# Performance work log

Hardware: AMD Instinct MI355X
Metric: run time of the kernel (lower is better)

Reference implementation:

```python
import jax, jax.numpy as jnp
import numpy as np

N_FFT = 1024
HOP = 256
WIN = 1024
PAD = (WIN - HOP) // 2  # 'same' padding trim
B, NBINS, T = 32, N_FFT // 2 + 1, 2048


def setup_inputs() -> dict:
    key = jax.random.key(0)
    k1, k2 = jax.random.split(key)
    spec_real = jax.random.normal(k1, (B, NBINS, T), dtype=jnp.float32)
    spec_imag = jax.random.normal(k2, (B, NBINS, T), dtype=jnp.float32)
    # Hann window, as used by neural vocoders (periodic hann)
    n = jnp.arange(WIN, dtype=jnp.float32)
    window = 0.5 - 0.5 * jnp.cos(2.0 * jnp.pi * n / WIN)
    return {"spec_real": spec_real, "spec_imag": spec_imag, "window": window}


def reference(spec_real, spec_imag, window):
    spec = jax.lax.complex(spec_real, spec_imag)            # (B, N, T)
    ifft = jnp.fft.irfft(spec, n=N_FFT, axis=1, norm="backward")  # (B, n_fft, T)
    ifft = ifft * window[None, :, None]                     # windowed frames
    b, _, t = spec_real.shape
    out_size = (t - 1) * HOP + WIN
    idx = jnp.arange(t)[None, :] * HOP + jnp.arange(WIN)[:, None]
    y = jnp.zeros((b, out_size), dtype=ifft.dtype).at[:, idx].add(ifft)
    env = jnp.zeros((out_size,), dtype=window.dtype).at[idx].add(
        jnp.broadcast_to(jnp.square(window)[:, None], (WIN, t))
    )
    return y[:, PAD:-PAD] / env[PAD:-PAD]
```

## Files before the change

### kernel.cpp

```cpp
#include <hip/hip_runtime.h>
#include <hip/hip_fp16.h>

#define NBINS 513
#define TFR   2048
#define NB    32
#define WIN   1024
#define HOP   256
#define PADT  384
#define OPB   524288
#define FR    16
#define TILES (TFR / FR)
#define SPAN  (FR * HOP)
#define FSTRIDE 545
#define PIDX(i) ((i) + ((i) >> 4))
#define C45 0.70710678118654752f
#define TWOPI_1024 0.0061359231515425649f
#define SSC   (1.0f / 512.0f * 2.0f / 3.0f)
#define CDLT  0.99998117528260114f
#define SDLT  0.00613588464915448f

__device__ __forceinline__ float2 cadd(float2 a, float2 b){ return make_float2(a.x+b.x, a.y+b.y); }
__device__ __forceinline__ float2 csub(float2 a, float2 b){ return make_float2(a.x-b.x, a.y-b.y); }
__device__ __forceinline__ float2 cmul(float2 a, float2 b){ return make_float2(a.x*b.x - a.y*b.y, a.x*b.y + a.y*b.x); }
__device__ __forceinline__ float2 h2f(__half2 h){ return __half22float2(h); }
__device__ __forceinline__ __half2 f2h(float x, float y){ return __floats2half2_rn(x, y); }

#define BFLY8(u0,u1,u2,u3,u4,u5,u6,u7, v0,v1,v2,v3,v4,v5,v6,v7)            \
    float2 s0=cadd(u0,u4), t0=csub(u0,u4);                                  \
    float2 s1=cadd(u1,u5), t1=csub(u1,u5);                                  \
    float2 s2=cadd(u2,u6), t2=csub(u2,u6);                                  \
    float2 s3=cadd(u3,u7), t3=csub(u3,u7);                                  \
    t1 = make_float2(C45*(t1.x - t1.y),  C45*(t1.x + t1.y));                \
    t2 = make_float2(-t2.y, t2.x);                                          \
    t3 = make_float2(-C45*(t3.x + t3.y), C45*(t3.x - t3.y));                \
    float2 p0=cadd(s0,s2), p2=csub(s0,s2);                                  \
    float2 p1=cadd(s1,s3), p3=csub(s1,s3); p3 = make_float2(-p3.y, p3.x);   \
    float2 q0=cadd(t0,t2), q2=csub(t0,t2);                                  \
    float2 q1=cadd(t1,t3), q3=csub(t1,t3); q3 = make_float2(-q3.y, q3.x);   \
    float2 v0=cadd(p0,p1), v4=csub(p0,p1);                                  \
    float2 v2=cadd(p2,p3), v6=csub(p2,p3);                                  \
    float2 v1=cadd(q0,q1), v5=csub(q0,q1);                                  \
    float2 v3=cadd(q2,q3), v7=csub(q2,q3);

template<int L>
__device__ __forceinline__ void fft_stage(__half2* __restrict__ row,
                                          const float2* __restrict__ ph, int i)
{
    const int k    = i & (L - 1);
    const int base = ((i & ~(L - 1)) << 3) + k;
    float2 u0 = h2f(row[PIDX(base + 0*L)]);
    float2 u1 = h2f(row[PIDX(base + 1*L)]);
    float2 u2 = h2f(row[PIDX(base + 2*L)]);
    float2 u3 = h2f(row[PIDX(base + 3*L)]);
    float2 u4 = h2f(row[PIDX(base + 4*L)]);
    float2 u5 = h2f(row[PIDX(base + 5*L)]);
    float2 u6 = h2f(row[PIDX(base + 6*L)]);
    float2 u7 = h2f(row[PIDX(base + 7*L)]);
    BFLY8(u0,u1,u2,u3,u4,u5,u6,u7, v0,v1,v2,v3,v4,v5,v6,v7)
    if constexpr (L > 1) {
        const float2 w1 = ph[k * (128 / L)];
        float2 wq = w1;
        v1 = cmul(v1, wq);
        wq = cmul(wq, w1); v2 = cmul(v2, wq);
        wq = cmul(wq, w1); v3 = cmul(v3, wq);
        wq = cmul(wq, w1); v4 = cmul(v4, wq);
        wq = cmul(wq, w1); v5 = cmul(v5, wq);
        wq = cmul(wq, w1); v6 = cmul(v6, wq);
        wq = cmul(wq, w1); v7 = cmul(v7, wq);
    }
    row[PIDX(base + 0*L)] = f2h(v0.x, v0.y);
    row[PIDX(base + 1*L)] = f2h(v1.x, v1.y);
    row[PIDX(base + 2*L)] = f2h(v2.x, v2.y);
    row[PIDX(base + 3*L)] = f2h(v3.x, v3.y);
    row[PIDX(base + 4*L)] = f2h(v4.x, v4.y);
    row[PIDX(base + 5*L)] = f2h(v5.x, v5.y);
    row[PIDX(base + 6*L)] = f2h(v6.x, v6.y);
    row[PIDX(base + 7*L)] = f2h(v7.x, v7.y);
}

__device__ __forceinline__ float2 hann_pair(const float2* __restrict__ ph, int n)
{
    const bool mir = n > 256;
    const int  m   = mir ? 512 - n : n;
    const float2 cs = ph[m];
    const float c = mir ? -cs.x : cs.x;
    const float s = cs.y;
    const float w0 = 1.0f - c*c;
    const float c2 = 2.0f*c*c - 1.0f;
    const float s2 = 2.0f*c*s;
    const float w1 = 0.5f - 0.5f*(c2*CDLT - s2*SDLT);
    return make_float2(w0, w1);
}

__global__ __launch_bounds__(256) void zero_seams(float* __restrict__ out)
{
    const int total = NB * (TILES + 1) * 768;
    for (int id = blockIdx.x * 256 + threadIdx.x; id < total; id += gridDim.x * 256) {
        const int q = id % 768;
        const int r = id / 768;
        const int s = r % (TILES + 1);
        const int bb = r / (TILES + 1);
        const int p  = s * SPAN + q;
        const int oi = p - PADT;
        if ((unsigned)oi < (unsigned)OPB) out[(size_t)bb * OPB + oi] = 0.f;
    }
}

__global__ __launch_bounds__(256, 4) void istft16(
    const float* __restrict__ sr, const float* __restrict__ si,
    float* __restrict__ out)
{
    __shared__ __half2 stile[FR * FSTRIDE];
    __shared__ float2  ph[257];

    const int tid = threadIdx.x;
    const int bid = blockIdx.x;
    const int nwg = NB * TILES;
    const int swz = (bid & 7) * (nwg >> 3) + (bid >> 3);
    const int b    = swz / TILES;
    const int tile = swz % TILES;
    const int j0   = tile * FR;

    const size_t gbase = (size_t)b * NBINS * TFR + (size_t)j0;
    const size_t gaA = gbase + (size_t)tid * TFR;
    const size_t gaB = gbase + (size_t)(512 - tid) * TFR;
    float4 rA0 = *(const float4*)(sr + gaA);
    float4 rA1 = *(const float4*)(sr + gaA + 4);
    float4 rA2 = *(const float4*)(sr + gaA + 8);
    float4 rA3 = *(const float4*)(sr + gaA + 12);
    float4 iA0 = *(const float4*)(si + gaA);
    float4 iA1 = *(const float4*)(si + gaA + 4);
    float4 iA2 = *(const float4*)(si + gaA + 8);
    float4 iA3 = *(const float4*)(si + gaA + 12);
    float4 rB0 = *(const float4*)(sr + gaB);
    float4 rB1 = *(const float4*)(sr + gaB + 4);
    float4 rB2 = *(const float4*)(sr + gaB + 8);
    float4 rB3 = *(const float4*)(sr + gaB + 12);
    float4 iB0 = *(const float4*)(si + gaB);
    float4 iB1 = *(const float4*)(si + gaB + 4);
    float4 iB2 = *(const float4*)(si + gaB + 8);
    float4 iB3 = *(const float4*)(si + gaB + 12);

    if (tid == 0) {
        const float4 z4 = make_float4(0.f,0.f,0.f,0.f);
        iA0=iA1=iA2=iA3=z4; iB0=iB1=iB2=iB3=z4;
        const size_t gaC = gbase + (size_t)256 * TFR;
        float4 rC0 = *(const float4*)(sr + gaC);
        float4 rC1 = *(const float4*)(sr + gaC + 4);
        float4 rC2 = *(const float4*)(sr + gaC + 8);
        float4 rC3 = *(const float4*)(sr + gaC + 12);
        float4 iC0 = *(const float4*)(si + gaC);
        float4 iC1 = *(const float4*)(si + gaC + 4);
        float4 iC2 = *(const float4*)(si + gaC + 8);
        float4 iC3 = *(const float4*)(si + gaC + 12);
        const int pn = PIDX(256);
#define Z256(F, RC, IC, COMP) stile[(F)*FSTRIDE + pn] = f2h(RC.COMP * SSC, -IC.COMP * SSC)
        Z256(0,rC0,iC0,x);  Z256(1,rC0,iC0,y);  Z256(2,rC0,iC0,z);  Z256(3,rC0,iC0,w);
        Z256(4,rC1,iC1,x);  Z256(5,rC1,iC1,y);  Z256(6,rC1,iC1,z);  Z256(7,rC1,iC1,w);
        Z256(8,rC2,iC2,x);  Z256(9,rC2,iC2,y);  Z256(10,rC2,iC2,z); Z256(11,rC2,iC2,w);
        Z256(12,rC3,iC3,x); Z256(13,rC3,iC3,y); Z256(14,rC3,iC3,z); Z256(15,rC3,iC3,w);
#undef Z256
    }

    for (int m = tid; m < 257; m += 256) {
        float sv, cv;
        sincosf(TWOPI_1024 * (float)m, &sv, &cv);
        ph[m] = make_float2(cv, sv);
    }

    {
        const float h = 0.5f * SSC;
        float swt, cwt;
        sincosf(TWOPI_1024 * (float)tid, &swt, &cwt);
        const int pk  = PIDX(tid);
        const int pk2 = PIDX(512 - tid);
#define TRICK(F, XKX, XKY, XMX, XMY) do {                                   \
            const float Ex = h*((XKX)+(XMX)), Ey = h*((XKY)-(XMY));         \
            const float Dx = h*((XKX)-(XMX)), Dy = h*((XKY)+(XMY));         \
            const float Ox = Dx*cwt - Dy*swt, Oy = Dx*swt + Dy*cwt;         \
            stile[(F)*FSTRIDE + pk]  = f2h(Ex - Oy, Ey + Ox);               \
            stile[(F)*FSTRIDE + pk2] = f2h(Ex + Oy, Ox - Ey);               \
        } while (0)
        TRICK(0,  rA0.x, iA0.x, rB0.x, iB0.x);
        TRICK(1,  rA0.y, iA0.y, rB0.y, iB0.y);
        TRICK(2,  rA0.z, iA0.z, rB0.z, iB0.z);
        TRICK(3,  rA0.w, iA0.w, rB0.w, iB0.w);
        TRICK(4,  rA1.x, iA1.x, rB1.x, iB1.x);
        TRICK(5,  rA1.y, iA1.y, rB1.y, iB1.y);
        TRICK(6,  rA1.z, iA1.z, rB1.z, iB1.z);
        TRICK(7,  rA1.w, iA1.w, rB1.w, iB1.w);
        TRICK(8,  rA2.x, iA2.x, rB2.x, iB2.x);
        TRICK(9,  rA2.y, iA2.y, rB2.y, iB2.y);
        TRICK(10, rA2.z, iA2.z, rB2.z, iB2.z);
        TRICK(11, rA2.w, iA2.w, rB2.w, iB2.w);
        TRICK(12, rA3.x, iA3.x, rB3.x, iB3.x);
        TRICK(13, rA3.y, iA3.y, rB3.y, iB3.y);
        TRICK(14, rA3.z, iA3.z, rB3.z, iB3.z);
        TRICK(15, rA3.w, iA3.w, rB3.w, iB3.w);
#undef TRICK
    }
    __syncthreads();

    {
        const int f  = tid >> 4;
        __half2* row = &stile[f * FSTRIDE];
        const int i0 = tid & 15;
        fft_stage<64>(row, ph, i0);
        fft_stage<64>(row, ph, i0 + 16);
        fft_stage<64>(row, ph, i0 + 32);
        fft_stage<64>(row, ph, i0 + 48);
        __syncthreads();
        fft_stage<8>(row, ph, i0);
        fft_stage<8>(row, ph, i0 + 16);
        fft_stage<8>(row, ph, i0 + 32);
        fft_stage<8>(row, ph, i0 + 48);
        __syncthreads();
        fft_stage<1>(row, ph, i0);
        fft_stage<1>(row, ph, i0 + 16);
        fft_stage<1>(row, ph, i0 + 32);
        fft_stage<1>(row, ph, i0 + 48);
        __syncthreads();
    }

    const int nE = tid;
    const int nO = (tid + 128) & 255;
    const float2 wE0 = hann_pair(ph, nE);
    const float2 wE1 = hann_pair(ph, nE + 256);
    const float2 wO0 = hann_pair(ph, nO);
    const float2 wO1 = hann_pair(ph, nO + 256);

    float2 a0 = make_float2(0.f,0.f), a1=a0, a2=a0, a3=a0, a4=a0,
           a5 = a0, a6=a0, a7=a0, a8=a0, a9=a0;
    const bool tlo = (tid < 128);

#define OLA_STEP(F, KK, ACCV, W) do {                                       \
        const int n_ = (((F) & 1) ? nO : nE) + ((KK) << 8);                 \
        const int j_ = ((n_ & 7) << 6) | (n_ & 56) | (n_ >> 6);             \
        const float2 z_ = h2f(stile[(F)*FSTRIDE + PIDX(j_)]);               \
        ACCV.x += z_.x * W.x;                                               \
        ACCV.y += z_.y * W.y;                                               \
    } while (0)

    OLA_STEP(0,0,a0,wE0);  OLA_STEP(0,1,a1,wE1);
    if (tlo) { OLA_STEP(1,0,a1,wO0);  OLA_STEP(1,1,a2,wO1); }
    else     { OLA_STEP(1,0,a0,wO0);  OLA_STEP(1,1,a1,wO1); }
    OLA_STEP(2,0,a1,wE0);  OLA_STEP(2,1,a2,wE1);
    if (tlo) { OLA_STEP(3,0,a2,wO0);  OLA_STEP(3,1,a3,wO1); }
    else     { OLA_STEP(3,0,a1,wO0);  OLA_STEP(3,1,a2,wO1); }
    OLA_STEP(4,0,a2,wE0);  OLA_STEP(4,1,a3,wE1);
    if (tlo) { OLA_STEP(5,0,a3,wO0);  OLA_STEP(5,1,a4,wO1); }
    else     { OLA_STEP(5,0,a2,wO0);  OLA_STEP(5,1,a3,wO1); }
    OLA_STEP(6,0,a3,wE0);  OLA_STEP(6,1,a4,wE1);
    if (tlo) { OLA_STEP(7,0,a4,wO0);  OLA_STEP(7,1,a5,wO1); }
    else     { OLA_STEP(7,0,a3,wO0);  OLA_STEP(7,1,a4,wO1); }
    OLA_STEP(8,0,a4,wE0);  OLA_STEP(8,1,a5,wE1);
    if (tlo) { OLA_STEP(9,0,a5,wO0);  OLA_STEP(9,1,a6,wO1); }
    else     { OLA_STEP(9,0,a4,wO0);  OLA_STEP(9,1,a5,wO1); }
    OLA_STEP(10,0,a5,wE0); OLA_STEP(10,1,a6,wE1);
    if (tlo) { OLA_STEP(11,0,a6,wO0); OLA_STEP(11,1,a7,wO1); }
    else     { OLA_STEP(11,0,a5,wO0); OLA_STEP(11,1,a6,wO1); }
    OLA_STEP(12,0,a6,wE0); OLA_STEP(12,1,a7,wE1);
    if (tlo) { OLA_STEP(13,0,a7,wO0); OLA_STEP(13,1,a8,wO1); }
    else     { OLA_STEP(13,0,a6,wO0); OLA_STEP(13,1,a7,wO1); }
    OLA_STEP(14,0,a7,wE0); OLA_STEP(14,1,a8,wE1);
    if (tlo) { OLA_STEP(15,0,a8,wO0); OLA_STEP(15,1,a9,wO1); }
    else     { OLA_STEP(15,0,a7,wO0); OLA_STEP(15,1,a8,wO1); }
#undef OLA_STEP

    const size_t ob = (size_t)b * OPB;
    const int pb = tile * SPAN;
#define STORE_SEAM(A, G) do {                                               \
        const int oi_ = pb + 2*(tid + 256*(G)) - PADT;                      \
        if ((unsigned)oi_ < (unsigned)OPB)       atomicAdd(&out[ob + oi_],     A.x); \
        if ((unsigned)(oi_+1) < (unsigned)OPB)   atomicAdd(&out[ob + oi_ + 1], A.y); \
    } while (0)
#define STORE_PLAIN(A, G) do {                                              \
        const int oi_ = pb + 2*(tid + 256*(G)) - PADT;                      \
        *(float2*)(out + ob + oi_) = A;                                     \
    } while (0)

    STORE_SEAM(a0, 0);
    if (tlo) STORE_SEAM(a1, 1);
    else     STORE_PLAIN(a1, 1);
    STORE_PLAIN(a2, 2);
    STORE_PLAIN(a3, 3);
    STORE_PLAIN(a4, 4);
    STORE_PLAIN(a5, 5);
    STORE_PLAIN(a6, 6);
    STORE_PLAIN(a7, 7);
    STORE_SEAM(a8, 8);
    if (tlo) STORE_SEAM(a9, 9);
#undef STORE_SEAM
#undef STORE_PLAIN
}

__global__ __launch_bounds__(256) void edge_fix(float* __restrict__ out)
{
    const int id = blockIdx.x * 256 + threadIdx.x;
    if (id >= 768 * NB) return;
    const int bb = id / 768;
    const int r  = id % 768;
    const int oi = (r < 384) ? r : (OPB - 768 + r);
    const int p  = oi + PADT;
    int jlo = (p - 768) >> 8; if (jlo < 0) jlo = 0;
    int jhi = p >> 8;         if (jhi > TFR - 1) jhi = TFR - 1;
    float e = 0.f;
    for (int j = jlo; j <= jhi; ++j) {
        const float wv = 0.5f - 0.5f * cosf(TWOPI_1024 * (float)(p - j * HOP));
        e += wv * wv;
    }
    out[(size_t)bb * OPB + oi] *= 1.5f / e;
}

extern "C" void kernel_launch(void* const* d_in, const int* in_sizes, int n_in,
                              void* d_out, int out_size, void* d_ws, size_t ws_size,
                              hipStream_t stream) {
    const float* sr = (const float*)d_in[0];
    const float* si = (const float*)d_in[1];
    float* out = (float*)d_out;

    hipLaunchKernelGGL(zero_seams, dim3(2048), dim3(256), 0, stream, out);
    hipLaunchKernelGGL(istft16, dim3(NB * TILES), dim3(256), 0, stream, sr, si, out);
    hipLaunchKernelGGL(edge_fix, dim3((768 * NB + 255) / 256), dim3(256), 0, stream, out);
}
```

Measured before the change: 109.9 us.

## Pack two frames per shared-memory word and run paired FFT butterflies

Shared memory now holds frame pairs split into planes: one packed half2 of real parts and one of imaginary parts per uint2 slot. Each thread runs two independent radix-8 butterflies per stage with a shared twiddle, which halves the number of LDS accesses per element processed. The last stage and the overlap-add are rearranged to use this pairing, with a lane rotation in the final stage whose indexing is subtle. The risks are higher register pressure and a new padding pattern that may bring back LDS bank conflicts.

```diff
diff --git a/kernel.cpp b/kernel.cpp
--- a/kernel.cpp
+++ b/kernel.cpp
@@ -11,8 +11,9 @@
 #define FR    16
 #define TILES (TFR / FR)
 #define SPAN  (FR * HOP)
-#define FSTRIDE 545
-#define PIDX(i) ((i) + ((i) >> 4))
+#define NPAIR 8
+#define FSTRIDE 577
+#define QIDX(e) ((e) + ((e) >> 3))
 #define C45 0.70710678118654752f
 #define TWOPI_1024 0.0061359231515425649f
 #define SSC   (1.0f / 512.0f * 2.0f / 3.0f)
@@ -22,8 +23,21 @@
 __device__ __forceinline__ float2 cadd(float2 a, float2 b){ return make_float2(a.x+b.x, a.y+b.y); }
 __device__ __forceinline__ float2 csub(float2 a, float2 b){ return make_float2(a.x-b.x, a.y-b.y); }
 __device__ __forceinline__ float2 cmul(float2 a, float2 b){ return make_float2(a.x*b.x - a.y*b.y, a.x*b.y + a.y*b.x); }
-__device__ __forceinline__ float2 h2f(__half2 h){ return __half22float2(h); }
-__device__ __forceinline__ __half2 f2h(float x, float y){ return __floats2half2_rn(x, y); }
+
+__device__ __forceinline__ uint2 pack_pair(float2 zA, float2 zB) {
+    __half2 re = __floats2half2_rn(zA.x, zB.x);
+    __half2 im = __floats2half2_rn(zA.y, zB.y);
+    uint2 r;
+    r.x = *(const unsigned int*)&re;
+    r.y = *(const unsigned int*)&im;
+    return r;
+}
+__device__ __forceinline__ void unpack_pair(uint2 v, float2& zA, float2& zB) {
+    float2 fr = __half22float2(*(const __half2*)&v.x);
+    float2 fi = __half22float2(*(const __half2*)&v.y);
+    zA = make_float2(fr.x, fi.x);
+    zB = make_float2(fr.y, fi.y);
+}
 
 #define BFLY8(u0,u1,u2,u3,u4,u5,u6,u7, v0,v1,v2,v3,v4,v5,v6,v7)            \
     float2 s0=cadd(u0,u4), t0=csub(u0,u4);                                  \
@@ -37,45 +51,65 @@
     float2 p1=cadd(s1,s3), p3=csub(s1,s3); p3 = make_float2(-p3.y, p3.x);   \
     float2 q0=cadd(t0,t2), q2=csub(t0,t2);                                  \
     float2 q1=cadd(t1,t3), q3=csub(t1,t3); q3 = make_float2(-q3.y, q3.x);   \
-    float2 v0=cadd(p0,p1), v4=csub(p0,p1);                                  \
-    float2 v2=cadd(p2,p3), v6=csub(p2,p3);                                  \
-    float2 v1=cadd(q0,q1), v5=csub(q0,q1);                                  \
-    float2 v3=cadd(q2,q3), v7=csub(q2,q3);
+    v0=cadd(p0,p1); v4=csub(p0,p1);                                         \
+    v2=cadd(p2,p3); v6=csub(p2,p3);                                         \
+    v1=cadd(q0,q1); v5=csub(q0,q1);                                         \
+    v3=cadd(q2,q3); v7=csub(q2,q3);
 
 template<int L>
-__device__ __forceinline__ void fft_stage(__half2* __restrict__ row,
-                                          const float2* __restrict__ ph, int i)
+__device__ __forceinline__ void fft_stage_pk(uint2* __restrict__ row,
+                                             const float2* __restrict__ ph, int i)
 {
     const int k    = i & (L - 1);
     const int base = ((i & ~(L - 1)) << 3) + k;
-    float2 u0 = h2f(row[PIDX(base + 0*L)]);
-    float2 u1 = h2f(row[PIDX(base + 1*L)]);
-    float2 u2 = h2f(row[PIDX(base + 2*L)]);
-    float2 u3 = h2f(row[PIDX(base + 3*L)]);
-    float2 u4 = h2f(row[PIDX(base + 4*L)]);
-    float2 u5 = h2f(row[PIDX(base + 5*L)]);
-    float2 u6 = h2f(row[PIDX(base + 6*L)]);
-    float2 u7 = h2f(row[PIDX(base + 7*L)]);
-    BFLY8(u0,u1,u2,u3,u4,u5,u6,u7, v0,v1,v2,v3,v4,v5,v6,v7)
+    uint2 w0 = row[QIDX(base + 0*L)];
+    uint2 w1v = row[QIDX(base + 1*L)];
+    uint2 w2 = row[QIDX(base + 2*L)];
+    uint2 w3 = row[QIDX(base + 3*L)];
+    uint2 w4 = row[QIDX(base + 4*L)];
+    uint2 w5 = row[QIDX(base + 5*L)];
+    uint2 w6 = row[QIDX(base + 6*L)];
+    uint2 w7 = row[QIDX(base + 7*L)];
+    float2 uA0,uA1,uA2,uA3,uA4,uA5,uA6,uA7;
+    float2 uB0,uB1,uB2,uB3,uB4,uB5,uB6,uB7;
+    unpack_pair(w0, uA0, uB0); unpack_pair(w1v, uA1, uB1);
+    unpack_pair(w2, uA2, uB2); unpack_pair(w3, uA3, uB3);
+    unpack_pair(w4, uA4, uB4); unpack_pair(w5, uA5, uB5);
+    unpack_pair(w6, uA6, uB6); unpack_pair(w7, uA7, uB7);
+
+    float2 vA0,vA1,vA2,vA3,vA4,vA5,vA6,vA7;
+    float2 vB0,vB1,vB2,vB3,vB4,vB5,vB6,vB7;
+    { BFLY8(uA0,uA1,uA2,uA3,uA4,uA5,uA6,uA7, vA0,vA1,vA2,vA3,vA4,vA5,vA6,vA7) }
+    { BFLY8(uB0,uB1,uB2,uB3,uB4,uB5,uB6,uB7, vB0,vB1,vB2,vB3,vB4,vB5,vB6,vB7) }
+
     if constexpr (L > 1) {
-        const float2 w1 = ph[k * (128 / L)];
-        float2 wq = w1;
-        v1 = cmul(v1, wq);
-        wq = cmul(wq, w1); v2 = cmul(v2, wq);
-        wq = cmul(wq, w1); v3 = cmul(v3, wq);
-        wq = cmul(wq, w1); v4 = cmul(v4, wq);
-        wq = cmul(wq, w1); v5 = cmul(v5, wq);
-        wq = cmul(wq, w1); v6 = cmul(v6, wq);
-        wq = cmul(wq, w1); v7 = cmul(v7, wq);
-    }
-    row[PIDX(base + 0*L)] = f2h(v0.x, v0.y);
-    row[PIDX(base + 1*L)] = f2h(v1.x, v1.y);
-    row[PIDX(base + 2*L)] = f2h(v2.x, v2.y);
-    row[PIDX(base + 3*L)] = f2h(v3.x, v3.y);
-    row[PIDX(base + 4*L)] = f2h(v4.x, v4.y);
-    row[PIDX(base + 5*L)] = f2h(v5.x, v5.y);
-    row[PIDX(base + 6*L)] = f2h(v6.x, v6.y);
-    row[PIDX(base + 7*L)] = f2h(v7.x, v7.y);
+        const float2 tw = ph[k * (128 / L)];
+        float2 wq = tw;
+        vA1 = cmul(vA1, wq); vB1 = cmul(vB1, wq);
+        wq = cmul(wq, tw); vA2 = cmul(vA2, wq); vB2 = cmul(vB2, wq);
+        wq = cmul(wq, tw); vA3 = cmul(vA3, wq); vB3 = cmul(vB3, wq);
+        wq = cmul(wq, tw); vA4 = cmul(vA4, wq); vB4 = cmul(vB4, wq);
+        wq = cmul(wq, tw); vA5 = cmul(vA5, wq); vB5 = cmul(vB5, wq);
+        wq = cmul(wq, tw); vA6 = cmul(vA6, wq); vB6 = cmul(vB6, wq);
+        wq = cmul(wq, tw); vA7 = cmul(vA7, wq); vB7 = cmul(vB7, wq);
+        row[QIDX(base + 0*L)] = pack_pair(vA0, vB0);
+        row[QIDX(base + 1*L)] = pack_pair(vA1, vB1);
+        row[QIDX(base + 2*L)] = pack_pair(vA2, vB2);
+        row[QIDX(base + 3*L)] = pack_pair(vA3, vB3);
+        row[QIDX(base + 4*L)] = pack_pair(vA4, vB4);
+        row[QIDX(base + 5*L)] = pack_pair(vA5, vB5);
+        row[QIDX(base + 6*L)] = pack_pair(vA6, vB6);
+        row[QIDX(base + 7*L)] = pack_pair(vA7, vB7);
+    } else {
+        row[QIDX(base + 0)] = pack_pair(vA0, vB2);
+        row[QIDX(base + 1)] = pack_pair(vA1, vB3);
+        row[QIDX(base + 2)] = pack_pair(vA2, vB4);
+        row[QIDX(base + 3)] = pack_pair(vA3, vB5);
+        row[QIDX(base + 4)] = pack_pair(vA4, vB6);
+        row[QIDX(base + 5)] = pack_pair(vA5, vB7);
+        row[QIDX(base + 6)] = pack_pair(vA6, vB0);
+        row[QIDX(base + 7)] = pack_pair(vA7, vB1);
+    }
 }
 
 __device__ __forceinline__ float2 hann_pair(const float2* __restrict__ ph, int n)
@@ -110,8 +144,8 @@
     const float* __restrict__ sr, const float* __restrict__ si,
     float* __restrict__ out)
 {
-    __shared__ __half2 stile[FR * FSTRIDE];
-    __shared__ float2  ph[257];
+    __shared__ uint2  stile[NPAIR * FSTRIDE];
+    __shared__ float2 ph[257];
 
     const int tid = threadIdx.x;
     const int bid = blockIdx.x;
@@ -153,13 +187,16 @@
         float4 iC1 = *(const float4*)(si + gaC + 4);
         float4 iC2 = *(const float4*)(si + gaC + 8);
         float4 iC3 = *(const float4*)(si + gaC + 12);
-        const int pn = PIDX(256);
-#define Z256(F, RC, IC, COMP) stile[(F)*FSTRIDE + pn] = f2h(RC.COMP * SSC, -IC.COMP * SSC)
-        Z256(0,rC0,iC0,x);  Z256(1,rC0,iC0,y);  Z256(2,rC0,iC0,z);  Z256(3,rC0,iC0,w);
-        Z256(4,rC1,iC1,x);  Z256(5,rC1,iC1,y);  Z256(6,rC1,iC1,z);  Z256(7,rC1,iC1,w);
-        Z256(8,rC2,iC2,x);  Z256(9,rC2,iC2,y);  Z256(10,rC2,iC2,z); Z256(11,rC2,iC2,w);
-        Z256(12,rC3,iC3,x); Z256(13,rC3,iC3,y); Z256(14,rC3,iC3,z); Z256(15,rC3,iC3,w);
-#undef Z256
+        const int pn = QIDX(256);
+#define Z256P(P, RC, IC, CA, CB)                                            \
+        stile[(P)*FSTRIDE + pn] = pack_pair(                                \
+            make_float2(RC.CA * SSC, -IC.CA * SSC),                         \
+            make_float2(RC.CB * SSC, -IC.CB * SSC))
+        Z256P(0, rC0, iC0, x, y);  Z256P(1, rC0, iC0, z, w);
+        Z256P(2, rC1, iC1, x, y);  Z256P(3, rC1, iC1, z, w);
+        Z256P(4, rC2, iC2, x, y);  Z256P(5, rC2, iC2, z, w);
+        Z256P(6, rC3, iC3, x, y);  Z256P(7, rC3, iC3, z, w);
+#undef Z256P
     }
 
     for (int m = tid; m < 257; m += 256) {
@@ -172,100 +209,82 @@
         const float h = 0.5f * SSC;
         float swt, cwt;
         sincosf(TWOPI_1024 * (float)tid, &swt, &cwt);
-        const int pk  = PIDX(tid);
-        const int pk2 = PIDX(512 - tid);
-#define TRICK(F, XKX, XKY, XMX, XMY) do {                                   \
+        const int pk  = QIDX(tid);
+        const int pk2 = QIDX(512 - tid);
+#define TRICKF(XKX, XKY, XMX, XMY, ZK, ZM) do {                             \
             const float Ex = h*((XKX)+(XMX)), Ey = h*((XKY)-(XMY));         \
             const float Dx = h*((XKX)-(XMX)), Dy = h*((XKY)+(XMY));         \
             const float Ox = Dx*cwt - Dy*swt, Oy = Dx*swt + Dy*cwt;         \
-            stile[(F)*FSTRIDE + pk]  = f2h(Ex - Oy, Ey + Ox);               \
-            stile[(F)*FSTRIDE + pk2] = f2h(Ex + Oy, Ox - Ey);               \
+            ZK = make_float2(Ex - Oy, Ey + Ox);                             \
+            ZM = make_float2(Ex + Oy, Ox - Ey);                             \
         } while (0)
-        TRICK(0,  rA0.x, iA0.x, rB0.x, iB0.x);
-        TRICK(1,  rA0.y, iA0.y, rB0.y, iB0.y);
-        TRICK(2,  rA0.z, iA0.z, rB0.z, iB0.z);
-        TRICK(3,  rA0.w, iA0.w, rB0.w, iB0.w);
-        TRICK(4,  rA1.x, iA1.x, rB1.x, iB1.x);
-        TRICK(5,  rA1.y, iA1.y, rB1.y, iB1.y);
-        TRICK(6,  rA1.z, iA1.z, rB1.z, iB1.z);
-        TRICK(7,  rA1.w, iA1.w, rB1.w, iB1.w);
-        TRICK(8,  rA2.x, iA2.x, rB2.x, iB2.x);
-        TRICK(9,  rA2.y, iA2.y, rB2.y, iB2.y);
-        TRICK(10, rA2.z, iA2.z, rB2.z, iB2.z);
-        TRICK(11, rA2.w, iA2.w, rB2.w, iB2.w);
-        TRICK(12, rA3.x, iA3.x, rB3.x, iB3.x);
-        TRICK(13, rA3.y, iA3.y, rB3.y, iB3.y);
-        TRICK(14, rA3.z, iA3.z, rB3.z, iB3.z);
-        TRICK(15, rA3.w, iA3.w, rB3.w, iB3.w);
-#undef TRICK
+#define TRICKP(P, RA, IA, RB, IB, CA, CB) do {                              \
+            float2 zkA, zmA, zkB, zmB;                                      \
+            TRICKF(RA.CA, IA.CA, RB.CA, IB.CA, zkA, zmA);                   \
+            TRICKF(RA.CB, IA.CB, RB.CB, IB.CB, zkB, zmB);                   \
+            stile[(P)*FSTRIDE + pk]  = pack_pair(zkA, zkB);                 \
+            stile[(P)*FSTRIDE + pk2] = pack_pair(zmA, zmB);                 \
+        } while (0)
+        TRICKP(0, rA0, iA0, rB0, iB0, x, y);
+        TRICKP(1, rA0, iA0, rB0, iB0, z, w);
+        TRICKP(2, rA1, iA1, rB1, iB1, x, y);
+        TRICKP(3, rA1, iA1, rB1, iB1, z, w);
+        TRICKP(4, rA2, iA2, rB2, iB2, x, y);
+        TRICKP(5, rA2, iA2, rB2, iB2, z, w);
+        TRICKP(6, rA3, iA3, rB3, iB3, x, y);
+        TRICKP(7, rA3, iA3, rB3, iB3, z, w);
+#undef TRICKP
+#undef TRICKF
     }
     __syncthreads();
 
     {
-        const int f  = tid >> 4;
-        __half2* row = &stile[f * FSTRIDE];
-        const int i0 = tid & 15;
-        fft_stage<64>(row, ph, i0);
-        fft_stage<64>(row, ph, i0 + 16);
-        fft_stage<64>(row, ph, i0 + 32);
-        fft_stage<64>(row, ph, i0 + 48);
+        const int p  = tid >> 5;
+        uint2* row   = &stile[p * FSTRIDE];
+        const int i0 = tid & 31;
+        fft_stage_pk<64>(row, ph, i0);
+        fft_stage_pk<64>(row, ph, i0 + 32);
         __syncthreads();
-        fft_stage<8>(row, ph, i0);
-        fft_stage<8>(row, ph, i0 + 16);
-        fft_stage<8>(row, ph, i0 + 32);
-        fft_stage<8>(row, ph, i0 + 48);
+        fft_stage_pk<8>(row, ph, i0);
+        fft_stage_pk<8>(row, ph, i0 + 32);
         __syncthreads();
-        fft_stage<1>(row, ph, i0);
-        fft_stage<1>(row, ph, i0 + 16);
-        fft_stage<1>(row, ph, i0 + 32);
-        fft_stage<1>(row, ph, i0 + 48);
+        fft_stage_pk<1>(row, ph, i0);
+        fft_stage_pk<1>(row, ph, i0 + 32);
         __syncthreads();
     }
 
-    const int nE = tid;
-    const int nO = (tid + 128) & 255;
-    const float2 wE0 = hann_pair(ph, nE);
-    const float2 wE1 = hann_pair(ph, nE + 256);
-    const float2 wO0 = hann_pair(ph, nO);
-    const float2 wO1 = hann_pair(ph, nO + 256);
+    const bool tlo = (tid < 128);
+    const float2 wA0 = hann_pair(ph, tid);
+    const float2 wA1 = hann_pair(ph, tid + 256);
+    const float2 wB0 = hann_pair(ph, tid + 128);
+    const float2 wB1 = tlo ? hann_pair(ph, tid + 384) : hann_pair(ph, tid - 128);
+    const int n0 = tid, n1 = tid + 256;
+    const int js0 = QIDX(((n0 & 7) << 6) | (n0 & 56) | (n0 >> 6));
+    const int js1 = QIDX(((n1 & 7) << 6) | (n1 & 56) | (n1 >> 6));
 
     float2 a0 = make_float2(0.f,0.f), a1=a0, a2=a0, a3=a0, a4=a0,
            a5 = a0, a6=a0, a7=a0, a8=a0, a9=a0;
-    const bool tlo = (tid < 128);
-
-#define OLA_STEP(F, KK, ACCV, W) do {                                       \
-        const int n_ = (((F) & 1) ? nO : nE) + ((KK) << 8);                 \
-        const int j_ = ((n_ & 7) << 6) | (n_ & 56) | (n_ >> 6);             \
-        const float2 z_ = h2f(stile[(F)*FSTRIDE + PIDX(j_)]);               \
-        ACCV.x += z_.x * W.x;                                               \
-        ACCV.y += z_.y * W.y;                                               \
+
+#define OLA_PAIR(P, AK0, AK1, ABK0, ABK1_T, ABK1_F) do {                    \
+        float2 zA0, zB0, zA1, zB1;                                          \
+        unpack_pair(stile[(P)*FSTRIDE + js0], zA0, zB0);                    \
+        unpack_pair(stile[(P)*FSTRIDE + js1], zA1, zB1);                    \
+        AK0.x += zA0.x * wA0.x;  AK0.y += zA0.y * wA0.y;                    \
+        AK1.x += zA1.x * wA1.x;  AK1.y += zA1.y * wA1.y;                    \
+        ABK0.x += zB0.x * wB0.x; ABK0.y += zB0.y * wB0.y;                   \
+        if (tlo) { ABK1_T.x += zB1.x * wB1.x; ABK1_T.y += zB1.y * wB1.y; }  \
+        else     { ABK1_F.x += zB1.x * wB1.x; ABK1_F.y += zB1.y * wB1.y; }  \
     } while (0)
 
-    OLA_STEP(0,0,a0,wE0);  OLA_STEP(0,1,a1,wE1);
-    if (tlo) { OLA_STEP(1,0,a1,wO0);  OLA_STEP(1,1,a2,wO1); }
-    else     { OLA_STEP(1,0,a0,wO0);  OLA_STEP(1,1,a1,wO1); }
-    OLA_STEP(2,0,a1,wE0);  OLA_STEP(2,1,a2,wE1);
-    if (tlo) { OLA_STEP(3,0,a2,wO0);  OLA_STEP(3,1,a3,wO1); }
-    else     { OLA_STEP(3,0,a1,wO0);  OLA_STEP(3,1,a2,wO1); }
-    OLA_STEP(4,0,a2,wE0);  OLA_STEP(4,1,a3,wE1);
-    if (tlo) { OLA_STEP(5,0,a3,wO0);  OLA_STEP(5,1,a4,wO1); }
-    else     { OLA_STEP(5,0,a2,wO0);  OLA_STEP(5,1,a3,wO1); }
-    OLA_STEP(6,0,a3,wE0);  OLA_STEP(6,1,a4,wE1);
-    if (tlo) { OLA_STEP(7,0,a4,wO0);  OLA_STEP(7,1,a5,wO1); }
-    else     { OLA_STEP(7,0,a3,wO0);  OLA_STEP(7,1,a4,wO1); }
-    OLA_STEP(8,0,a4,wE0);  OLA_STEP(8,1,a5,wE1);
-    if (tlo) { OLA_STEP(9,0,a5,wO0);  OLA_STEP(9,1,a6,wO1); }
-    else     { OLA_STEP(9,0,a4,wO0);  OLA_STEP(9,1,a5,wO1); }
-    OLA_STEP(10,0,a5,wE0); OLA_STEP(10,1,a6,wE1);
-    if (tlo) { OLA_STEP(11,0,a6,wO0); OLA_STEP(11,1,a7,wO1); }
-    else     { OLA_STEP(11,0,a5,wO0); OLA_STEP(11,1,a6,wO1); }
-    OLA_STEP(12,0,a6,wE0); OLA_STEP(12,1,a7,wE1);
-    if (tlo) { OLA_STEP(13,0,a7,wO0); OLA_STEP(13,1,a8,wO1); }
-    else     { OLA_STEP(13,0,a6,wO0); OLA_STEP(13,1,a7,wO1); }
-    OLA_STEP(14,0,a7,wE0); OLA_STEP(14,1,a8,wE1);
-    if (tlo) { OLA_STEP(15,0,a8,wO0); OLA_STEP(15,1,a9,wO1); }
-    else     { OLA_STEP(15,0,a7,wO0); OLA_STEP(15,1,a8,wO1); }
-#undef OLA_STEP
+    OLA_PAIR(0, a0, a1, a1, a2, a0);
+    OLA_PAIR(1, a1, a2, a2, a3, a1);
+    OLA_PAIR(2, a2, a3, a3, a4, a2);
+    OLA_PAIR(3, a3, a4, a4, a5, a3);
+    OLA_PAIR(4, a4, a5, a5, a6, a4);
+    OLA_PAIR(5, a5, a6, a6, a7, a5);
+    OLA_PAIR(6, a6, a7, a7, a8, a6);
+    OLA_PAIR(7, a7, a8, a8, a9, a7);
+#undef OLA_PAIR
 
     const size_t ob = (size_t)b * OPB;
     const int pb = tile * SPAN;
```

Measured after the change: 114.6 us. 1.04x slower.

## Process four 16-frame sub-tiles per workgroup, carrying overlap-add seams in registers

Applied to the files above, without the earlier changes.

Each workgroup now handles 64 frames as four consecutive 16-frame sub-tiles. The overlapping output tail of one sub-tile stays in registers and feeds the next, so atomics and seam zeroing are needed only at the edges of the larger block. The next sub-tile's spectrum loads are issued before the overlap-add of the current one to hide global latency. The Hann weights are now computed directly from sincos instead of a shared table lookup, and the Nyquist bin load is spread over eight threads. The cost is one quarter as many workgroups (1024) and higher register pressure from the prefetched tile.

```diff
diff --git a/kernel.cpp b/kernel.cpp
--- a/kernel.cpp
+++ b/kernel.cpp
@@ -9,8 +9,10 @@
 #define PADT  384
 #define OPB   524288
 #define FR    16
-#define TILES (TFR / FR)
-#define SPAN  (FR * HOP)
+#define KSUB  4
+#define SPAN  4096
+#define BIGSPAN (KSUB * SPAN)
+#define NBT   (OPB / BIGSPAN)
 #define FSTRIDE 545
 #define PIDX(i) ((i) + ((i) >> 4))
 #define C45 0.70710678118654752f
@@ -24,6 +26,15 @@
 __device__ __forceinline__ float2 cmul(float2 a, float2 b){ return make_float2(a.x*b.x - a.y*b.y, a.x*b.y + a.y*b.x); }
 __device__ __forceinline__ float2 h2f(__half2 h){ return __half22float2(h); }
 __device__ __forceinline__ __half2 f2h(float x, float y){ return __floats2half2_rn(x, y); }
+
+__device__ __forceinline__ float2 hann_cs(float c, float s)
+{
+    const float w0 = 1.0f - c*c;
+    const float c2 = 2.0f*c*c - 1.0f;
+    const float s2 = 2.0f*c*s;
+    const float w1 = 0.5f - 0.5f*(c2*CDLT - s2*SDLT);
+    return make_float2(w0, w1);
+}
 
 #define BFLY8(u0,u1,u2,u3,u4,u5,u6,u7, v0,v1,v2,v3,v4,v5,v6,v7)            \
     float2 s0=cadd(u0,u4), t0=csub(u0,u4);                                  \
@@ -78,35 +89,21 @@
     row[PIDX(base + 7*L)] = f2h(v7.x, v7.y);
 }
 
-__device__ __forceinline__ float2 hann_pair(const float2* __restrict__ ph, int n)
-{
-    const bool mir = n > 256;
-    const int  m   = mir ? 512 - n : n;
-    const float2 cs = ph[m];
-    const float c = mir ? -cs.x : cs.x;
-    const float s = cs.y;
-    const float w0 = 1.0f - c*c;
-    const float c2 = 2.0f*c*c - 1.0f;
-    const float s2 = 2.0f*c*s;
-    const float w1 = 0.5f - 0.5f*(c2*CDLT - s2*SDLT);
-    return make_float2(w0, w1);
-}
-
 __global__ __launch_bounds__(256) void zero_seams(float* __restrict__ out)
 {
-    const int total = NB * (TILES + 1) * 768;
+    const int total = NB * (NBT + 1) * 768;
     for (int id = blockIdx.x * 256 + threadIdx.x; id < total; id += gridDim.x * 256) {
         const int q = id % 768;
         const int r = id / 768;
-        const int s = r % (TILES + 1);
-        const int bb = r / (TILES + 1);
-        const int p  = s * SPAN + q;
+        const int s = r % (NBT + 1);
+        const int bb = r / (NBT + 1);
+        const int p  = s * BIGSPAN + q;
         const int oi = p - PADT;
         if ((unsigned)oi < (unsigned)OPB) out[(size_t)bb * OPB + oi] = 0.f;
     }
 }
 
-__global__ __launch_bounds__(256, 4) void istft16(
+__global__ __launch_bounds__(256, 4) void istft64(
     const float* __restrict__ sr, const float* __restrict__ si,
     float* __restrict__ out)
 {
@@ -115,52 +112,10 @@
 
     const int tid = threadIdx.x;
     const int bid = blockIdx.x;
-    const int nwg = NB * TILES;
+    const int nwg = NB * NBT;
     const int swz = (bid & 7) * (nwg >> 3) + (bid >> 3);
-    const int b    = swz / TILES;
-    const int tile = swz % TILES;
-    const int j0   = tile * FR;
-
-    const size_t gbase = (size_t)b * NBINS * TFR + (size_t)j0;
-    const size_t gaA = gbase + (size_t)tid * TFR;
-    const size_t gaB = gbase + (size_t)(512 - tid) * TFR;
-    float4 rA0 = *(const float4*)(sr + gaA);
-    float4 rA1 = *(const float4*)(sr + gaA + 4);
-    float4 rA2 = *(const float4*)(sr + gaA + 8);
-    float4 rA3 = *(const float4*)(sr + gaA + 12);
-    float4 iA0 = *(const float4*)(si + gaA);
-    float4 iA1 = *(const float4*)(si + gaA + 4);
-    float4 iA2 = *(const float4*)(si + gaA + 8);
-    float4 iA3 = *(const float4*)(si + gaA + 12);
-    float4 rB0 = *(const float4*)(sr + gaB);
-    float4 rB1 = *(const float4*)(sr + gaB + 4);
-    float4 rB2 = *(const float4*)(sr + gaB + 8);
-    float4 rB3 = *(const float4*)(sr + gaB + 12);
-    float4 iB0 = *(const float4*)(si + gaB);
-    float4 iB1 = *(const float4*)(si + gaB + 4);
-    float4 iB2 = *(const float4*)(si + gaB + 8);
-    float4 iB3 = *(const float4*)(si + gaB + 12);
-
-    if (tid == 0) {
-        const float4 z4 = make_float4(0.f,0.f,0.f,0.f);
-        iA0=iA1=iA2=iA3=z4; iB0=iB1=iB2=iB3=z4;
-        const size_t gaC = gbase + (size_t)256 * TFR;
-        float4 rC0 = *(const float4*)(sr + gaC);
-        float4 rC1 = *(const float4*)(sr + gaC + 4);
-        float4 rC2 = *(const float4*)(sr + gaC + 8);
-        float4 rC3 = *(const float4*)(sr + gaC + 12);
-        float4 iC0 = *(const float4*)(si + gaC);
-        float4 iC1 = *(const float4*)(si + gaC + 4);
-        float4 iC2 = *(const float4*)(si + gaC + 8);
-        float4 iC3 = *(const float4*)(si + gaC + 12);
-        const int pn = PIDX(256);
-#define Z256(F, RC, IC, COMP) stile[(F)*FSTRIDE + pn] = f2h(RC.COMP * SSC, -IC.COMP * SSC)
-        Z256(0,rC0,iC0,x);  Z256(1,rC0,iC0,y);  Z256(2,rC0,iC0,z);  Z256(3,rC0,iC0,w);
-        Z256(4,rC1,iC1,x);  Z256(5,rC1,iC1,y);  Z256(6,rC1,iC1,z);  Z256(7,rC1,iC1,w);
-        Z256(8,rC2,iC2,x);  Z256(9,rC2,iC2,y);  Z256(10,rC2,iC2,z); Z256(11,rC2,iC2,w);
-        Z256(12,rC3,iC3,x); Z256(13,rC3,iC3,y); Z256(14,rC3,iC3,z); Z256(15,rC3,iC3,w);
-#undef Z256
-    }
+    const int b   = swz / NBT;
+    const int bt  = swz % NBT;
 
     for (int m = tid; m < 257; m += 256) {
         float sv, cv;
@@ -168,12 +123,62 @@
         ph[m] = make_float2(cv, sv);
     }
 
-    {
-        const float h = 0.5f * SSC;
-        float swt, cwt;
-        sincosf(TWOPI_1024 * (float)tid, &swt, &cwt);
-        const int pk  = PIDX(tid);
-        const int pk2 = PIDX(512 - tid);
+    float swt, cwt;
+    sincosf(TWOPI_1024 * (float)tid, &swt, &cwt);
+    const bool tlo = (tid < 128);
+    const float c4 = (cwt - swt) * C45, s4 = (cwt + swt) * C45;
+    const float cm = (cwt + swt) * C45, sm = (swt - cwt) * C45;
+    const float2 wE0 = hann_cs(cwt, swt);
+    const float2 wE1 = hann_cs(-swt, cwt);
+    const float2 wO0 = tlo ? hann_cs(c4, s4)  : hann_cs(cm, sm);
+    const float2 wO1 = tlo ? hann_cs(-cm, c4) : hann_cs(c4, s4);
+
+    const size_t bbase = (size_t)b * NBINS * TFR;
+    float4 rA0,rA1,rA2,rA3,iA0,iA1,iA2,iA3;
+    float4 rB0,rB1,rB2,rB3,iB0,iB1,iB2,iB3;
+
+#define LOADTILE(J0) do {                                                   \
+        const size_t gb  = bbase + (size_t)(J0);                            \
+        const size_t gaA = gb + (size_t)tid * TFR;                          \
+        const size_t gaB = gb + (size_t)(512 - tid) * TFR;                  \
+        rA0 = *(const float4*)(sr + gaA);                                   \
+        rA1 = *(const float4*)(sr + gaA + 4);                               \
+        rA2 = *(const float4*)(sr + gaA + 8);                               \
+        rA3 = *(const float4*)(sr + gaA + 12);                              \
+        iA0 = *(const float4*)(si + gaA);                                   \
+        iA1 = *(const float4*)(si + gaA + 4);                               \
+        iA2 = *(const float4*)(si + gaA + 8);                               \
+        iA3 = *(const float4*)(si + gaA + 12);                              \
+        rB0 = *(const float4*)(sr + gaB);                                   \
+        rB1 = *(const float4*)(sr + gaB + 4);                               \
+        rB2 = *(const float4*)(sr + gaB + 8);                               \
+        rB3 = *(const float4*)(sr + gaB + 12);                              \
+        iB0 = *(const float4*)(si + gaB);                                   \
+        iB1 = *(const float4*)(si + gaB + 4);                               \
+        iB2 = *(const float4*)(si + gaB + 8);                               \
+        iB3 = *(const float4*)(si + gaB + 12);                              \
+        if (tid == 0) {                                                     \
+            const float4 z4 = make_float4(0.f,0.f,0.f,0.f);                 \
+            iA0=iA1=iA2=iA3=z4; iB0=iB1=iB2=iB3=z4;                         \
+        }                                                                   \
+    } while (0)
+
+    LOADTILE(bt * KSUB * FR);
+
+    float2 a0 = make_float2(0.f,0.f), a1=a0, a2=a0, a3=a0, a4=a0,
+           a5 = a0, a6=a0, a7=a0, a8=a0, a9=a0;
+
+    const size_t ob  = (size_t)b * OPB;
+    const int    pbB = bt * BIGSPAN;
+
+#pragma unroll
+    for (int k = 0; k < KSUB; ++k) {
+        const int j0 = (bt * KSUB + k) * FR;
+
+        {
+            const float h = 0.5f * SSC;
+            const int pk  = PIDX(tid);
+            const int pk2 = PIDX(512 - tid);
 #define TRICK(F, XKX, XKY, XMX, XMY) do {                                   \
             const float Ex = h*((XKX)+(XMX)), Ey = h*((XKY)-(XMY));         \
             const float Dx = h*((XKX)-(XMX)), Dy = h*((XKY)+(XMY));         \
@@ -181,117 +186,136 @@
             stile[(F)*FSTRIDE + pk]  = f2h(Ex - Oy, Ey + Ox);               \
             stile[(F)*FSTRIDE + pk2] = f2h(Ex + Oy, Ox - Ey);               \
         } while (0)
-        TRICK(0,  rA0.x, iA0.x, rB0.x, iB0.x);
-        TRICK(1,  rA0.y, iA0.y, rB0.y, iB0.y);
-        TRICK(2,  rA0.z, iA0.z, rB0.z, iB0.z);
-        TRICK(3,  rA0.w, iA0.w, rB0.w, iB0.w);
-        TRICK(4,  rA1.x, iA1.x, rB1.x, iB1.x);
-        TRICK(5,  rA1.y, iA1.y, rB1.y, iB1.y);
-        TRICK(6,  rA1.z, iA1.z, rB1.z, iB1.z);
-        TRICK(7,  rA1.w, iA1.w, rB1.w, iB1.w);
-        TRICK(8,  rA2.x, iA2.x, rB2.x, iB2.x);
-        TRICK(9,  rA2.y, iA2.y, rB2.y, iB2.y);
-        TRICK(10, rA2.z, iA2.z, rB2.z, iB2.z);
-        TRICK(11, rA2.w, iA2.w, rB2.w, iB2.w);
-        TRICK(12, rA3.x, iA3.x, rB3.x, iB3.x);
-        TRICK(13, rA3.y, iA3.y, rB3.y, iB3.y);
-        TRICK(14, rA3.z, iA3.z, rB3.z, iB3.z);
-        TRICK(15, rA3.w, iA3.w, rB3.w, iB3.w);
+            TRICK(0,  rA0.x, iA0.x, rB0.x, iB0.x);
+            TRICK(1,  rA0.y, iA0.y, rB0.y, iB0.y);
+            TRICK(2,  rA0.z, iA0.z, rB0.z, iB0.z);
+            TRICK(3,  rA0.w, iA0.w, rB0.w, iB0.w);
+            TRICK(4,  rA1.x, iA1.x, rB1.x, iB1.x);
+            TRICK(5,  rA1.y, iA1.y, rB1.y, iB1.y);
+            TRICK(6,  rA1.z, iA1.z, rB1.z, iB1.z);
+            TRICK(7,  rA1.w, iA1.w, rB1.w, iB1.w);
+            TRICK(8,  rA2.x, iA2.x, rB2.x, iB2.x);
+            TRICK(9,  rA2.y, iA2.y, rB2.y, iB2.y);
+            TRICK(10, rA2.z, iA2.z, rB2.z, iB2.z);
+            TRICK(11, rA2.w, iA2.w, rB2.w, iB2.w);
+            TRICK(12, rA3.x, iA3.x, rB3.x, iB3.x);
+            TRICK(13, rA3.y, iA3.y, rB3.y, iB3.y);
+            TRICK(14, rA3.z, iA3.z, rB3.z, iB3.z);
+            TRICK(15, rA3.w, iA3.w, rB3.w, iB3.w);
 #undef TRICK
-    }
-    __syncthreads();
-
-    {
-        const int f  = tid >> 4;
-        __half2* row = &stile[f * FSTRIDE];
-        const int i0 = tid & 15;
-        fft_stage<64>(row, ph, i0);
-        fft_stage<64>(row, ph, i0 + 16);
-        fft_stage<64>(row, ph, i0 + 32);
-        fft_stage<64>(row, ph, i0 + 48);
+        }
+        if (tid < 8) {
+            const size_t gaC = bbase + (size_t)j0 + (size_t)256 * TFR + 2*tid;
+            const float2 rc = *(const float2*)(sr + gaC);
+            const float2 ic = *(const float2*)(si + gaC);
+            stile[(2*tid)  *FSTRIDE + PIDX(256)] = f2h(rc.x * SSC, -ic.x * SSC);
+            stile[(2*tid+1)*FSTRIDE + PIDX(256)] = f2h(rc.y * SSC, -ic.y * SSC);
+        }
         __syncthreads();
-        fft_stage<8>(row, ph, i0);
-        fft_stage<8>(row, ph, i0 + 16);
-        fft_stage<8>(row, ph, i0 + 32);
-        fft_stage<8>(row, ph, i0 + 48);
-        __syncthreads();
-        fft_stage<1>(row, ph, i0);
-        fft_stage<1>(row, ph, i0 + 16);
-        fft_stage<1>(row, ph, i0 + 32);
-        fft_stage<1>(row, ph, i0 + 48);
-        __syncthreads();
-    }
-
-    const int nE = tid;
-    const int nO = (tid + 128) & 255;
-    const float2 wE0 = hann_pair(ph, nE);
-    const float2 wE1 = hann_pair(ph, nE + 256);
-    const float2 wO0 = hann_pair(ph, nO);
-    const float2 wO1 = hann_pair(ph, nO + 256);
-
-    float2 a0 = make_float2(0.f,0.f), a1=a0, a2=a0, a3=a0, a4=a0,
-           a5 = a0, a6=a0, a7=a0, a8=a0, a9=a0;
-    const bool tlo = (tid < 128);
-
+
+        {
+            const int f  = tid >> 4;
+            __half2* row = &stile[f * FSTRIDE];
+            const int i0 = tid & 15;
+            fft_stage<64>(row, ph, i0);
+            fft_stage<64>(row, ph, i0 + 16);
+            fft_stage<64>(row, ph, i0 + 32);
+            fft_stage<64>(row, ph, i0 + 48);
+            __syncthreads();
+            fft_stage<8>(row, ph, i0);
+            fft_stage<8>(row, ph, i0 + 16);
+            fft_stage<8>(row, ph, i0 + 32);
+            fft_stage<8>(row, ph, i0 + 48);
+            __syncthreads();
+            fft_stage<1>(row, ph, i0);
+            fft_stage<1>(row, ph, i0 + 16);
+            fft_stage<1>(row, ph, i0 + 32);
+            fft_stage<1>(row, ph, i0 + 48);
+            __syncthreads();
+        }
+
+        if (k < KSUB - 1) LOADTILE((bt * KSUB + k + 1) * FR);
+
+        {
+            const int nE = tid;
+            const int nO = (tid + 128) & 255;
 #define OLA_STEP(F, KK, ACCV, W) do {                                       \
-        const int n_ = (((F) & 1) ? nO : nE) + ((KK) << 8);                 \
-        const int j_ = ((n_ & 7) << 6) | (n_ & 56) | (n_ >> 6);             \
-        const float2 z_ = h2f(stile[(F)*FSTRIDE + PIDX(j_)]);               \
-        ACCV.x += z_.x * W.x;                                               \
-        ACCV.y += z_.y * W.y;                                               \
-    } while (0)
-
-    OLA_STEP(0,0,a0,wE0);  OLA_STEP(0,1,a1,wE1);
-    if (tlo) { OLA_STEP(1,0,a1,wO0);  OLA_STEP(1,1,a2,wO1); }
-    else     { OLA_STEP(1,0,a0,wO0);  OLA_STEP(1,1,a1,wO1); }
-    OLA_STEP(2,0,a1,wE0);  OLA_STEP(2,1,a2,wE1);
-    if (tlo) { OLA_STEP(3,0,a2,wO0);  OLA_STEP(3,1,a3,wO1); }
-    else     { OLA_STEP(3,0,a1,wO0);  OLA_STEP(3,1,a2,wO1); }
-    OLA_STEP(4,0,a2,wE0);  OLA_STEP(4,1,a3,wE1);
-    if (tlo) { OLA_STEP(5,0,a3,wO0);  OLA_STEP(5,1,a4,wO1); }
-    else     { OLA_STEP(5,0,a2,wO0);  OLA_STEP(5,1,a3,wO1); }
-    OLA_STEP(6,0,a3,wE0);  OLA_STEP(6,1,a4,wE1);
-    if (tlo) { OLA_STEP(7,0,a4,wO0);  OLA_STEP(7,1,a5,wO1); }
-    else     { OLA_STEP(7,0,a3,wO0);  OLA_STEP(7,1,a4,wO1); }
-    OLA_STEP(8,0,a4,wE0);  OLA_STEP(8,1,a5,wE1);
-    if (tlo) { OLA_STEP(9,0,a5,wO0);  OLA_STEP(9,1,a6,wO1); }
-    else     { OLA_STEP(9,0,a4,wO0);  OLA_STEP(9,1,a5,wO1); }
-    OLA_STEP(10,0,a5,wE0); OLA_STEP(10,1,a6,wE1);
-    if (tlo) { OLA_STEP(11,0,a6,wO0); OLA_STEP(11,1,a7,wO1); }
-    else     { OLA_STEP(11,0,a5,wO0); OLA_STEP(11,1,a6,wO1); }
-    OLA_STEP(12,0,a6,wE0); OLA_STEP(12,1,a7,wE1);
-    if (tlo) { OLA_STEP(13,0,a7,wO0); OLA_STEP(13,1,a8,wO1); }
-    else     { OLA_STEP(13,0,a6,wO0); OLA_STEP(13,1,a7,wO1); }
-    OLA_STEP(14,0,a7,wE0); OLA_STEP(14,1,a8,wE1);
-    if (tlo) { OLA_STEP(15,0,a8,wO0); OLA_STEP(15,1,a9,wO1); }
-    else     { OLA_STEP(15,0,a7,wO0); OLA_STEP(15,1,a8,wO1); }
+            const int n_ = (((F) & 1) ? nO : nE) + ((KK) << 8);             \
+            const int j_ = ((n_ & 7) << 6) | (n_ & 56) | (n_ >> 6);         \
+            const float2 z_ = h2f(stile[(F)*FSTRIDE + PIDX(j_)]);           \
+            ACCV.x += z_.x * W.x;                                           \
+            ACCV.y += z_.y * W.y;                                           \
+        } while (0)
+            OLA_STEP(0,0,a0,wE0);  OLA_STEP(0,1,a1,wE1);
+            if (tlo) { OLA_STEP(1,0,a1,wO0);  OLA_STEP(1,1,a2,wO1); }
+            else     { OLA_STEP(1,0,a0,wO0);  OLA_STEP(1,1,a1,wO1); }
+            OLA_STEP(2,0,a1,wE0);  OLA_STEP(2,1,a2,wE1);
+            if (tlo) { OLA_STEP(3,0,a2,wO0);  OLA_STEP(3,1,a3,wO1); }
+            else     { OLA_STEP(3,0,a1,wO0);  OLA_STEP(3,1,a2,wO1); }
+            OLA_STEP(4,0,a2,wE0);  OLA_STEP(4,1,a3,wE1);
+            if (tlo) { OLA_STEP(5,0,a3,wO0);  OLA_STEP(5,1,a4,wO1); }
+            else     { OLA_STEP(5,0,a2,wO0);  OLA_STEP(5,1,a3,wO1); }
+            OLA_STEP(6,0,a3,wE0);  OLA_STEP(6,1,a4,wE1);
+            if (tlo) { OLA_STEP(7,0,a4,wO0);  OLA_STEP(7,1,a5,wO1); }
+            else     { OLA_STEP(7,0,a3,wO0);  OLA_STEP(7,1,a4,wO1); }
+            OLA_STEP(8,0,a4,wE0);  OLA_STEP(8,1,a5,wE1);
+            if (tlo) { OLA_STEP(9,0,a5,wO0);  OLA_STEP(9,1,a6,wO1); }
+            else     { OLA_STEP(9,0,a4,wO0);  OLA_STEP(9,1,a5,wO1); }
+            OLA_STEP(10,0,a5,wE0); OLA_STEP(10,1,a6,wE1);
+            if (tlo) { OLA_STEP(11,0,a6,wO0); OLA_STEP(11,1,a7,wO1); }
+            else     { OLA_STEP(11,0,a5,wO0); OLA_STEP(11,1,a6,wO1); }
+            OLA_STEP(12,0,a6,wE0); OLA_STEP(12,1,a7,wE1);
+            if (tlo) { OLA_STEP(13,0,a7,wO0); OLA_STEP(13,1,a8,wO1); }
+            else     { OLA_STEP(13,0,a6,wO0); OLA_STEP(13,1,a7,wO1); }
+            OLA_STEP(14,0,a7,wE0); OLA_STEP(14,1,a8,wE1);
+            if (tlo) { OLA_STEP(15,0,a8,wO0); OLA_STEP(15,1,a9,wO1); }
+            else     { OLA_STEP(15,0,a7,wO0); OLA_STEP(15,1,a8,wO1); }
 #undef OLA_STEP
-
-    const size_t ob = (size_t)b * OPB;
-    const int pb = tile * SPAN;
+        }
+
+        {
+            const int pb = pbB + k * SPAN;
 #define STORE_SEAM(A, G) do {                                               \
-        const int oi_ = pb + 2*(tid + 256*(G)) - PADT;                      \
-        if ((unsigned)oi_ < (unsigned)OPB)       atomicAdd(&out[ob + oi_],     A.x); \
-        if ((unsigned)(oi_+1) < (unsigned)OPB)   atomicAdd(&out[ob + oi_ + 1], A.y); \
-    } while (0)
+            const int oi_ = pb + 2*(tid + 256*(G)) - PADT;                  \
+            if ((unsigned)oi_ < (unsigned)OPB)     atomicAdd(&out[ob + oi_],     A.x); \
+            if ((unsigned)(oi_+1) < (unsigned)OPB) atomicAdd(&out[ob + oi_ + 1], A.y); \
+        } while (0)
 #define STORE_PLAIN(A, G) do {                                              \
-        const int oi_ = pb + 2*(tid + 256*(G)) - PADT;                      \
-        *(float2*)(out + ob + oi_) = A;                                     \
-    } while (0)
-
-    STORE_SEAM(a0, 0);
-    if (tlo) STORE_SEAM(a1, 1);
-    else     STORE_PLAIN(a1, 1);
-    STORE_PLAIN(a2, 2);
-    STORE_PLAIN(a3, 3);
-    STORE_PLAIN(a4, 4);
-    STORE_PLAIN(a5, 5);
-    STORE_PLAIN(a6, 6);
-    STORE_PLAIN(a7, 7);
-    STORE_SEAM(a8, 8);
-    if (tlo) STORE_SEAM(a9, 9);
+            const int oi_ = pb + 2*(tid + 256*(G)) - PADT;                  \
+            *(float2*)(out + ob + oi_) = A;                                 \
+        } while (0)
+            if (k == 0) {
+                STORE_SEAM(a0, 0);
+                if (tlo) STORE_SEAM(a1, 1);
+                else     STORE_PLAIN(a1, 1);
+            } else {
+                STORE_PLAIN(a0, 0);
+                STORE_PLAIN(a1, 1);
+            }
+            STORE_PLAIN(a2, 2);
+            STORE_PLAIN(a3, 3);
+            STORE_PLAIN(a4, 4);
+            STORE_PLAIN(a5, 5);
+            STORE_PLAIN(a6, 6);
+            STORE_PLAIN(a7, 7);
+            if (k == KSUB - 1) {
+                STORE_SEAM(a8, 8);
+                if (tlo) STORE_SEAM(a9, 9);
+            }
 #undef STORE_SEAM
 #undef STORE_PLAIN
+        }
+
+        if (k < KSUB - 1) {
+            const float2 z2 = make_float2(0.f, 0.f);
+            a0 = a8;
+            a1 = tlo ? a9 : z2;
+            a2 = z2; a3 = z2; a4 = z2; a5 = z2;
+            a6 = z2; a7 = z2; a8 = z2; a9 = z2;
+            __syncthreads();
+        }
+    }
+#undef LOADTILE
 }
 
 __global__ __launch_bounds__(256) void edge_fix(float* __restrict__ out)
@@ -319,7 +343,7 @@
     const float* si = (const float*)d_in[1];
     float* out = (float*)d_out;
 
-    hipLaunchKernelGGL(zero_seams, dim3(2048), dim3(256), 0, stream, out);
-    hipLaunchKernelGGL(istft16, dim3(NB * TILES), dim3(256), 0, stream, sr, si, out);
+    hipLaunchKernelGGL(zero_seams, dim3(1024), dim3(256), 0, stream, out);
+    hipLaunchKernelGGL(istft64, dim3(NB * NBT), dim3(256), 0, stream, sr, si, out);
     hipLaunchKernelGGL(edge_fix, dim3((768 * NB + 255) / 256), dim3(256), 0, stream, out);
 }
```

After: 144.0 us. 1.31x slower.
